# Kernel tuning notes

Measured on AMD Instinct MI355X. Metric: run time of the kernel, lower is better.

The kernel has to match this reference:

```python
import jax, jax.numpy as jnp
import numpy as np

KSIZE = 11
SIGMA = 1.5
PAD = KSIZE // 2
C1 = 0.01 ** 2
C2 = 0.03 ** 2


def gaussian_kernel(ksize, sigma):
    ax = np.arange(ksize, dtype=np.float32) - (ksize - 1) / 2.0
    g = np.exp(-(ax ** 2) / (2.0 * sigma ** 2))
    k2d = np.outer(g, g)
    k2d = k2d / k2d.sum()
    # depthwise kernel for 3 channels: [out=3, in/groups=1, kh, kw]
    return jnp.asarray(np.broadcast_to(k2d, (3, 1, ksize, ksize)).copy())


def dwconv(x, kernel):
    # x: [B,3,H,W], kernel: [3,1,k,k], 'same' padding, groups=3
    return jax.lax.conv_general_dilated(
        x, kernel,
        window_strides=(1, 1),
        padding=[(PAD, PAD), (PAD, PAD)],
        dimension_numbers=('NCHW', 'OIHW', 'NCHW'),
        feature_group_count=3)


def setup_inputs() -> dict:
    key = jax.random.key(0)
    k1, k2 = jax.random.split(key)
    shape = (16, 3, 512, 512)
    img_output = jax.random.uniform(k1, shape, dtype=jnp.float32)
    img_target = jax.random.uniform(k2, shape, dtype=jnp.float32)
    kernel = gaussian_kernel(KSIZE, SIGMA)
    return {"img_output": img_output, "img_target": img_target, "kernel": kernel}


def reference(img_output, img_target, kernel):
    s, t = img_output, img_target
    ux = dwconv(s, kernel)
    uy = dwconv(t, kernel)
    uxx = dwconv(s * s, kernel)
    uyy = dwconv(t * t, kernel)
    uxy = dwconv(s * t, kernel)
    ssim = ((2 * ux * uy + C1) * (2 * (uxy - ux * uy) + C2)
            / (ux ** 2 + uy ** 2 + C1)
            / (uxx - ux * ux + (uyy - uy * uy) + C2))
    return 1.0 - ssim.mean()
```

## Files before the change

### kernel.cpp

```cpp
#include <hip/hip_runtime.h>

typedef _Float16 f16;
typedef f16  f16x8 __attribute__((ext_vector_type(8)));
typedef f16  f16x4 __attribute__((ext_vector_type(4)));
typedef f16  f16x2 __attribute__((ext_vector_type(2)));
typedef float f32x4 __attribute__((ext_vector_type(4)));

#define W 512
#define H 512
#define KS 11
#define NW 4
#define NBLK 3072
#define NLINES 256
#define C1_SSIM 0.0001f
#define C2_SSIM 0.0009f
#define NTOTAL 12582912.0f

__device__ __constant__ const float GW[KS] = {
    1.02838e-3f, 7.59876e-3f, 3.600076e-2f, 1.0936069e-1f, 2.1300554e-1f,
    2.6601172e-1f,
    2.1300554e-1f, 1.0936069e-1f, 3.600076e-2f, 7.59876e-3f, 1.02838e-3f
};

__device__ inline float ssim_px(float ux, float uy, float uxx, float uyy, float uxy) {
    const float uxuy = ux * uy;
    const float a = 2.f * uxuy + C1_SSIM;
    const float b = 2.f * (uxy - uxuy) + C2_SSIM;
    const float c = ux * ux + uy * uy + C1_SSIM;
    const float d = (uxx - ux * ux) + (uyy - uy * uy) + C2_SSIM;
    return (a * b) * __builtin_amdgcn_rcpf(c * d);
}

struct __attribute__((aligned(4))) F4 { float x, y, z, w; };

__device__ __forceinline__ void load8f(const float* __restrict__ base, int ry,
                                       int xs, float v[8]) {
    if ((unsigned)ry < (unsigned)H) {
        const float* r = base + ((size_t)ry << 9);
        if ((unsigned)xs <= (unsigned)(W - 8)) {
            const F4 a = *(const F4*)(r + xs);
            const F4 b = *(const F4*)(r + xs + 4);
            v[0] = a.x; v[1] = a.y; v[2] = a.z; v[3] = a.w;
            v[4] = b.x; v[5] = b.y; v[6] = b.z; v[7] = b.w;
        } else {
            #pragma unroll
            for (int j = 0; j < 8; ++j) {
                const int x = xs + j;
                v[j] = ((unsigned)x < (unsigned)W) ? r[x] : 0.f;
            }
        }
    } else {
        #pragma unroll
        for (int j = 0; j < 8; ++j) v[j] = 0.f;
    }
}

__device__ __forceinline__ f16x8 pack8(const float v[8]) {
    f16x8 r;
    #pragma unroll
    for (int p = 0; p < 4; ++p) {
        const f16x2 h = __builtin_bit_cast(
            f16x2, __builtin_amdgcn_cvt_pkrtz(v[2 * p], v[2 * p + 1]));
        r[2 * p]     = h[0];
        r[2 * p + 1] = h[1];
    }
    return r;
}

__global__ __launch_bounds__(256, 4)
void ssim_main(const float* __restrict__ simg, const float* __restrict__ timg,
               float* __restrict__ accum) {
    __shared__ float red[NW];

    const int tid  = threadIdx.x;
    const int w    = tid >> 6;
    const int lane = tid & 63;
    const int n    = lane & 15;
    const int q    = lane >> 4;

    const int L  = blockIdx.x * NW + w;
    const int z  = L >> 8;
    const int r  = L & 255;
    const int ty = r >> 5;
    const int tx = r & 31;

    const float* sp = simg + ((size_t)z << 18);
    const float* tp = timg + ((size_t)z << 18);
    const int x0 = tx << 4;
    const int y0 = (ty << 6) - 5;
    const int xs = x0 - 5 + (q << 3);

    float va[5][8], vb[5][8];
    #pragma unroll
    for (int g = 0; g < 5; ++g) {
        load8f(sp, y0 + (g << 4) + n, xs, va[g]);
        load8f(tp, y0 + (g << 4) + n, xs, vb[g]);
    }

    f16x8 af;
    #pragma unroll
    for (int j = 0; j < 8; ++j) {
        const int k = (q << 3) + j;
        const int d = k - n;
        af[j] = (d >= 0 && d < KS) ? (f16)GW[d] : (f16)0.f;
    }

    f16x4 a1v, a2v;
    #pragma unroll
    for (int j = 0; j < 4; ++j) {
        const int k  = (q << 2) + j;
        const int d1 = k - n;
        const int d2 = k + 16 - n;
        a1v[j] = (d1 >= 0 && d1 < KS) ? (f16)GW[d1] : (f16)0.f;
        a2v[j] = (d2 >= 0 && d2 < KS) ? (f16)GW[d2] : (f16)0.f;
    }

    union H4 { f16x4 v4; f16x2 v2[2]; };

    f16x4 ph[2][5];
    float sum = 0.f;

    #pragma unroll
    for (int g = 0; g < 5; ++g) {
        const int pb = g & 1;
        const f16x8 sf = pack8(va[g]);
        const f16x8 tf = pack8(vb[g]);
        #pragma unroll
        for (int c = 0; c < 5; ++c) {
            f16x8 ch;
            if      (c == 0) ch = sf;
            else if (c == 1) ch = tf;
            else if (c == 2) ch = sf * sf;
            else if (c == 3) ch = tf * tf;
            else             ch = sf * tf;
            const f32x4 zero = {0.f, 0.f, 0.f, 0.f};
            const f32x4 d = __builtin_amdgcn_mfma_f32_16x16x32_f16(ch, af, zero, 0, 0, 0);
            H4 u;
            u.v2[0] = __builtin_bit_cast(f16x2, __builtin_amdgcn_cvt_pkrtz(d[0], d[1]));
            u.v2[1] = __builtin_bit_cast(f16x2, __builtin_amdgcn_cvt_pkrtz(d[2], d[3]));
            ph[pb][c] = u.v4;
        }
        if (g >= 1) {
            const int pa = pb ^ 1;
            f32x4 acc[5];
            #pragma unroll
            for (int c = 0; c < 5; ++c) {
                const f32x4 zero = {0.f, 0.f, 0.f, 0.f};
                f32x4 a = __builtin_amdgcn_mfma_f32_16x16x16f16(a2v, ph[pb][c], zero, 0, 0, 0);
                a = __builtin_amdgcn_mfma_f32_16x16x16f16(a1v, ph[pa][c], a, 0, 0, 0);
                acc[c] = a;
            }
            #pragma unroll
            for (int rg = 0; rg < 4; ++rg)
                sum += ssim_px(acc[0][rg], acc[1][rg], acc[2][rg],
                               acc[3][rg], acc[4][rg]);
        }
    }

    #pragma unroll
    for (int off = 32; off > 0; off >>= 1)
        sum += __shfl_down(sum, off, 64);
    if (lane == 0) red[w] = sum;
    __syncthreads();
    if (tid == 0) {
        atomicAdd(&accum[(blockIdx.x & (NLINES - 1)) << 4],
                  red[0] + red[1] + red[2] + red[3]);
    }
}

__global__ void ssim_final(const float* __restrict__ accum, float* __restrict__ out) {
    const int lane = threadIdx.x;
    float s = 0.f;
    #pragma unroll
    for (int i = 0; i < NLINES / 64; ++i)
        s += accum[((i << 6) + lane) << 4];
    #pragma unroll
    for (int off = 32; off > 0; off >>= 1)
        s += __shfl_down(s, off, 64);
    if (lane == 0) out[0] = 1.f - s * (1.f / NTOTAL);
}

extern "C" void kernel_launch(void* const* d_in, const int* in_sizes, int n_in,
                              void* d_out, int out_size, void* d_ws, size_t ws_size,
                              hipStream_t stream) {
    const float* s = (const float*)d_in[0];
    const float* t = (const float*)d_in[1];
    float* out   = (float*)d_out;
    float* accum = (float*)d_ws;

    hipMemsetAsync(accum, 0, NLINES * 16 * sizeof(float), stream);
    ssim_main<<<dim3(NBLK), 256, 0, stream>>>(s, t, accum);
    ssim_final<<<1, 64, 0, stream>>>(accum, out);
}
```

Baseline: 160.4 us.

## Stage 64x64 tiles of both images in LDS as fp16 to share halos across waves

Each block now handles a 64x64 output tile instead of four separate 16x64 strips. It cooperatively loads the haloed 80x80 region of both images once, converts it to fp16 and stores it in shared memory. Each wave then reads its 16-column slice from LDS, so horizontal halo loads are no longer repeated across neighbouring waves. The horizontal weight offset is shifted to match the 8-aligned LDS window, and launch bounds are raised to 6 blocks per CU. The trade-off is a __syncthreads, about 25 KB of LDS per block, and less memory-level parallelism per wave.

```diff
diff --git a/kernel.cpp b/kernel.cpp
--- a/kernel.cpp
+++ b/kernel.cpp
@@ -16,6 +16,9 @@
 #define C2_SSIM 0.0009f
 #define NTOTAL 12582912.0f
 
+#define LROWS 80
+#define LSTRIDE 80
+
 __device__ __constant__ const float GW[KS] = {
     1.02838e-3f, 7.59876e-3f, 3.600076e-2f, 1.0936069e-1f, 2.1300554e-1f,
     2.6601172e-1f,
@@ -31,29 +34,7 @@
     return (a * b) * __builtin_amdgcn_rcpf(c * d);
 }
 
-struct __attribute__((aligned(4))) F4 { float x, y, z, w; };
-
-__device__ __forceinline__ void load8f(const float* __restrict__ base, int ry,
-                                       int xs, float v[8]) {
-    if ((unsigned)ry < (unsigned)H) {
-        const float* r = base + ((size_t)ry << 9);
-        if ((unsigned)xs <= (unsigned)(W - 8)) {
-            const F4 a = *(const F4*)(r + xs);
-            const F4 b = *(const F4*)(r + xs + 4);
-            v[0] = a.x; v[1] = a.y; v[2] = a.z; v[3] = a.w;
-            v[4] = b.x; v[5] = b.y; v[6] = b.z; v[7] = b.w;
-        } else {
-            #pragma unroll
-            for (int j = 0; j < 8; ++j) {
-                const int x = xs + j;
-                v[j] = ((unsigned)x < (unsigned)W) ? r[x] : 0.f;
-            }
-        }
-    } else {
-        #pragma unroll
-        for (int j = 0; j < 8; ++j) v[j] = 0.f;
-    }
-}
+struct __attribute__((aligned(16))) F4 { float x, y, z, w; };
 
 __device__ __forceinline__ f16x8 pack8(const float v[8]) {
     f16x8 r;
@@ -67,9 +48,10 @@
     return r;
 }
 
-__global__ __launch_bounds__(256, 4)
+__global__ __launch_bounds__(256, 6)
 void ssim_main(const float* __restrict__ simg, const float* __restrict__ timg,
                float* __restrict__ accum) {
+    __shared__ __align__(16) f16 lds[2][LROWS * LSTRIDE];
     __shared__ float red[NW];
 
     const int tid  = threadIdx.x;
@@ -78,33 +60,53 @@
     const int n    = lane & 15;
     const int q    = lane >> 4;
 
-    const int L  = blockIdx.x * NW + w;
-    const int z  = L >> 8;
-    const int r  = L & 255;
-    const int ty = r >> 5;
-    const int tx = r & 31;
+    const int bid = blockIdx.x;
+    const int z   = bid >> 6;
+    const int rr  = bid & 63;
+    const int ty  = rr >> 3;
+    const int tx  = rr & 7;
 
     const float* sp = simg + ((size_t)z << 18);
     const float* tp = timg + ((size_t)z << 18);
-    const int x0 = tx << 4;
-    const int y0 = (ty << 6) - 5;
-    const int xs = x0 - 5 + (q << 3);
-
-    float va[5][8], vb[5][8];
-    #pragma unroll
-    for (int g = 0; g < 5; ++g) {
-        load8f(sp, y0 + (g << 4) + n, xs, va[g]);
-        load8f(tp, y0 + (g << 4) + n, xs, vb[g]);
+    const int x0    = tx << 6;
+    const int ybase = (ty << 6) - 5;
+    const int xbase = x0 - 8;
+
+    #pragma unroll
+    for (int it = 0; it < 7; ++it) {
+        const int t = it * 256 + tid;
+        if (it < 6 || t < 1600) {
+            const int img = (t >= 800) ? 1 : 0;
+            const int u   = img ? (t - 800) : t;
+            const int lr  = (u * 205) >> 11;
+            const int sg  = u - lr * 10;
+            const int ry  = ybase + lr;
+            const int cx  = xbase + (sg << 3);
+            const float* src = img ? tp : sp;
+            float v[8];
+            const bool ok = ((unsigned)ry < (unsigned)H) &
+                            ((unsigned)cx <= (unsigned)(W - 8));
+            if (ok) {
+                const float* rp = src + ((size_t)ry << 9) + cx;
+                const F4 a = *(const F4*)rp;
+                const F4 b = *(const F4*)(rp + 4);
+                v[0] = a.x; v[1] = a.y; v[2] = a.z; v[3] = a.w;
+                v[4] = b.x; v[5] = b.y; v[6] = b.z; v[7] = b.w;
+            } else {
+                #pragma unroll
+                for (int j = 0; j < 8; ++j) v[j] = 0.f;
+            }
+            *(f16x8*)&lds[img][lr * LSTRIDE + (sg << 3)] = pack8(v);
+        }
     }
 
     f16x8 af;
     #pragma unroll
     for (int j = 0; j < 8; ++j) {
         const int k = (q << 3) + j;
-        const int d = k - n;
+        const int d = k - n - 3;
         af[j] = (d >= 0 && d < KS) ? (f16)GW[d] : (f16)0.f;
     }
-
     f16x4 a1v, a2v;
     #pragma unroll
     for (int j = 0; j < 4; ++j) {
@@ -115,16 +117,22 @@
         a2v[j] = (d2 >= 0 && d2 < KS) ? (f16)GW[d2] : (f16)0.f;
     }
 
+    __syncthreads();
+
     union H4 { f16x4 v4; f16x2 v2[2]; };
+    const int coff = (w << 4) + (q << 3);
+    const f16* lss = &lds[0][coff];
+    const f16* lts = &lds[1][coff];
 
     f16x4 ph[2][5];
     float sum = 0.f;
 
     #pragma unroll
     for (int g = 0; g < 5; ++g) {
+        const int rowoff = ((g << 4) + n) * LSTRIDE;
+        const f16x8 sf = *(const f16x8*)(lss + rowoff);
+        const f16x8 tf = *(const f16x8*)(lts + rowoff);
         const int pb = g & 1;
-        const f16x8 sf = pack8(va[g]);
-        const f16x8 tf = pack8(vb[g]);
         #pragma unroll
         for (int c = 0; c < 5; ++c) {
             f16x8 ch;
```

Measured after the change: 139.1 us. -13.3%, faster.
